# Performance work log

Measured on AMD Instinct MI355X. Metric: run time of the kernel, lower is better.

The kernel has to match this reference:

```python
import jax, jax.numpy as jnp
import numpy as np

N = 384      # max_nodes
H = 256      # layers[0] == layers[1] == layers[2]
Z = 128      # dim_z
ED = 128     # edge_dim
AH = ED // 2 # attention hidden

# complete directed graph: combinations (i<j) then reversed pairs
_i, _j = np.triu_indices(N, k=1)
_SRC = jnp.asarray(np.concatenate([_i, _j]), dtype=jnp.int32)  # edge_index[0]
_DST = jnp.asarray(np.concatenate([_j, _i]), dtype=jnp.int32)  # edge_index[1]


def setup_inputs() -> dict:
    key = jax.random.key(0)
    ks = jax.random.split(key, 16)
    def p(k, shape, fan_in):
        return jax.random.normal(k, shape, dtype=jnp.float32) * (1.0 / np.sqrt(fan_in))
    return {
        "z": jax.random.normal(ks[0], (1, Z), dtype=jnp.float32),
        # GRU (torch layout: W_ih [3H, Z], W_hh [3H, H]; gate order r, z, n)
        "gru_Wih": p(ks[1], (3 * H, Z), Z),
        "gru_Whh": p(ks[2], (3 * H, H), H),
        "gru_bih": jnp.zeros((3 * H,), jnp.float32),
        "gru_bhh": jnp.zeros((3 * H,), jnp.float32),
        # edge_generator MLP: 2H -> 4H -> ED
        "eg_W1": p(ks[3], (2 * H, 4 * H), 2 * H), "eg_b1": jnp.zeros((4 * H,), jnp.float32),
        "eg_W2": p(ks[4], (4 * H, ED), 4 * H),   "eg_b2": jnp.zeros((ED,), jnp.float32),
        # attention MLPs: (ED+H) -> ED//2 -> 1
        "att0_W1": p(ks[5], (ED + H, AH), ED + H), "att0_b1": jnp.zeros((AH,), jnp.float32),
        "att0_W2": p(ks[6], (AH, 1), AH),           "att0_b2": jnp.zeros((1,), jnp.float32),
        "att1_W1": p(ks[7], (ED + H, AH), ED + H), "att1_b1": jnp.zeros((AH,), jnp.float32),
        "att1_W2": p(ks[8], (AH, 1), AH),           "att1_b2": jnp.zeros((1,), jnp.float32),
        # EdgeConv output linears: H -> H
        "conv0_W": p(ks[9], (H, H), H),  "conv0_b": jnp.zeros((H,), jnp.float32),
        "conv1_W": p(ks[10], (H, H), H), "conv1_b": jnp.zeros((H,), jnp.float32),
    }


def _forward(z, gru_Wih, gru_Whh, gru_bih, gru_bhh,
             eg_W1, eg_b1, eg_W2, eg_b2,
             att0_W1, att0_b1, att0_W2, att0_b2,
             att1_W1, att1_b1, att1_W2, att1_b2,
             conv0_W, conv0_b, conv1_W, conv1_b):
    # --- GRU node generation: input is the same latent z at every step ---
    gi = z[0] @ gru_Wih.T + gru_bih            # [3H], constant per step
    gir, giz, gin = jnp.split(gi, 3)
    def step(h, _):
        gh = h @ gru_Whh.T + gru_bhh
        ghr, ghz, ghn = jnp.split(gh, 3)
        r = jax.nn.sigmoid(gir + ghr)
        u = jax.nn.sigmoid(giz + ghz)
        n = jnp.tanh(gin + r * ghn)
        h2 = (1.0 - u) * n + u * h
        return h2, h2
    _, nodes = jax.lax.scan(step, jnp.zeros((H,), z.dtype), None, length=N)  # [N, H]

    # --- edge features over the complete directed graph ---
    pairs = jnp.concatenate([nodes[_SRC], nodes[_DST]], axis=-1)            # [E, 2H]
    edges = jax.nn.relu(pairs @ eg_W1 + eg_b1) @ eg_W2 + eg_b2              # [E, ED]

    # --- EdgeConv: gather src, attention MLP gate, scatter-sum, linear ---
    def conv(x, aW1, ab1, aW2, ab2, W, b):
        xs = x[_SRC]                                                        # [E, H]
        a_in = jnp.concatenate([edges, xs], axis=-1)                        # [E, ED+H]
        att = jax.nn.sigmoid(jax.nn.relu(a_in @ aW1 + ab1) @ aW2 + ab2)     # [E, 1]
        agg = jax.ops.segment_sum(att * xs, _DST, num_segments=N)           # [N, H]
        return agg @ W + b

    x = jax.nn.relu(conv(nodes, att0_W1, att0_b1, att0_W2, att0_b2, conv0_W, conv0_b))
    x = conv(x, att1_W1, att1_b1, att1_W2, att1_b2, conv1_W, conv1_b)
    return jnp.sum(x, axis=0)                                               # [H]


def reference(z, gru_Wih, gru_Whh, gru_bih, gru_bhh,
              eg_W1, eg_b1, eg_W2, eg_b2,
              att0_W1, att0_b1, att0_W2, att0_b2,
              att1_W1, att1_b1, att1_W2, att1_b2,
              conv0_W, conv0_b, conv1_W, conv1_b):
    return _forward(z, gru_Wih, gru_Whh, gru_bih, gru_bhh,
                    eg_W1, eg_b1, eg_W2, eg_b2,
                    att0_W1, att0_b1, att0_W2, att0_b2,
                    att1_W1, att1_b1, att1_W2, att1_b2,
                    conv0_W, conv0_b, conv1_W, conv1_b)
```

## Files before the change

### kernel.cpp

```cpp
#include <hip/hip_runtime.h>
#include <hip/hip_fp16.h>
#include <cstdint>

#define DEV static __device__ __forceinline__

typedef _Float16 h2v __attribute__((ext_vector_type(2)));
typedef _Float16 half8 __attribute__((ext_vector_type(8)));
typedef float float4v __attribute__((ext_vector_type(4)));

union U32H2 { uint32_t u; _Float16 f[2]; };

DEV uint32_t pack_f2(float a, float b) {
    auto p = __builtin_amdgcn_cvt_pkrtz(a, b);
    return __builtin_bit_cast(uint32_t, p);
}

DEV half8 bc8(uint4 v) { return __builtin_bit_cast(half8, v); }

DEV void gl_lds16(const void* gsrc, void* ldst) {
    __builtin_amdgcn_global_load_lds(
        (const __attribute__((address_space(1))) uint32_t*)gsrc,
        (__attribute__((address_space(3))) uint32_t*)ldst, 16, 0, 0);
}

DEV float pick4(float4v lo, float4v hi, int bsel, int r) {
    float v0 = bsel ? hi[0] : lo[0];
    float v1 = bsel ? hi[1] : lo[1];
    float v2 = bsel ? hi[2] : lo[2];
    float v3 = bsel ? hi[3] : lo[3];
    float x01 = (r & 1) ? v1 : v0;
    float x23 = (r & 1) ? v3 : v2;
    return (r & 2) ? x23 : x01;
}

static const size_t OFF_W16T  = 0;
static const size_t OFF_GI    = 98304;
static const size_t OFF_CC    = 99072;
static const size_t OFF_BF    = 99200;
static const size_t OFF_NODES = 164736;
static const size_t OFF_PF    = 263040;
static const size_t OFF_QF    = 459648;
static const size_t OFF_R0    = 656256;
static const size_t OFF_R1    = 680832;
static const size_t OFF_TT    = 705408;
static const size_t OFF_ATT0  = 10142592;
static const size_t OFF_ATT1  = 10290048;
static const size_t OFF_AGG   = 10437504;
static const size_t OFF_X0    = 10535808;
static const size_t OFF_CS    = 10634112;
static const size_t WS_TOTAL  = 10634816;

__global__ void k_prep_wl(const float* __restrict__ Whh, uint32_t* __restrict__ WL,
                          const float* __restrict__ z, const float* __restrict__ Wih,
                          const float* __restrict__ bih, const float* __restrict__ bhh,
                          float* __restrict__ gs) {
    int bb = blockIdx.x, tid = threadIdx.x;
    if (bb < 48) {
        int c = bb;
        int rt = c >> 3, kt = c & 7;
        int lane = tid & 63, wv = tid >> 6;
        int row = (rt >> 1) * 256 + wv * 32 + ((rt & 1) << 4) + (lane & 15);
        int k0 = kt*32 + (lane >> 4)*8;
        const float* src = Whh + row*256 + k0;
        uint4 o;
        o.x = pack_f2(src[0], src[1]);
        o.y = pack_f2(src[2], src[3]);
        o.z = pack_f2(src[4], src[5]);
        o.w = pack_f2(src[6], src[7]);
        ((uint4*)WL)[c*512 + tid] = o;
    } else {
        int o = (bb - 48) * 512 + tid;
        if (o < 768) {
            float acc = bih[o];
            if (o < 512) acc += bhh[o];
            for (int i = 0; i < 128; ++i) acc += Wih[o*128 + i] * z[i];
            gs[o] = acc;
        }
    }
}

__global__ void __launch_bounds__(512, 2)
k_gru_bf(const float* __restrict__ gs, const float* __restrict__ bhh,
         const uint32_t* __restrict__ WL, float* __restrict__ nodes,
         const float* __restrict__ egW2, const float* __restrict__ egb2,
         const float* __restrict__ a0W1, const float* __restrict__ a1W1,
         uint32_t* __restrict__ BF, float* __restrict__ cc) {
    int bb = blockIdx.x, tid = threadIdx.x;
    if (bb == 0) {
        __shared__ __align__(16) _Float16 hh16[512];
        int lane = tid & 63, wv = tid >> 6;
        int kq = lane >> 4, c = lane & 15;
        const float L2E = 1.44269504088896f;
        int r = c & 3, bsel = (c >> 2) & 1;
        int gidx = wv*32 + kq*4 + r + bsel*16;
        bool active = (c < 8);

        uint4 w[48];
        const uint4* wl4 = (const uint4*)WL;
        #pragma unroll
        for (int q = 0; q < 48; ++q) w[q] = wl4[q*512 + tid];
        #pragma unroll
        for (int q = 0; q < 48; ++q)
            asm volatile("" : "+a"(w[q].x), "+a"(w[q].y), "+a"(w[q].z), "+a"(w[q].w));

        float pr = -L2E * gs[gidx];
        float pz = -L2E * gs[256 + gidx];
        float pn = -2.f * L2E * gs[512 + gidx];
        float bn_l = bhh[512 + gidx];

        float h = 0.f;
        if (tid < 256) ((uint32_t*)hh16)[tid] = 0u;
        __syncthreads();

        const float4v z4 = {0.f, 0.f, 0.f, 0.f};
        int par = 0;
        for (int t = 0; t < 384; ++t) {
            const _Float16* hb = hh16 + par*256 + kq*8;
            uint4 b[8];
            #pragma unroll
            for (int kt = 0; kt < 8; ++kt) b[kt] = *(const uint4*)(hb + kt*32);

            float4v d0, d1, d2, d3, d4, d5;
            d0 = __builtin_amdgcn_mfma_f32_16x16x32_f16(bc8(w[0]),  bc8(b[0]), z4, 0, 0, 0);
            d1 = __builtin_amdgcn_mfma_f32_16x16x32_f16(bc8(w[8]),  bc8(b[0]), z4, 0, 0, 0);
            #pragma unroll
            for (int kt = 1; kt < 8; ++kt) {
                d0 = __builtin_amdgcn_mfma_f32_16x16x32_f16(bc8(w[kt]),   bc8(b[kt]), d0, 0, 0, 0);
                d1 = __builtin_amdgcn_mfma_f32_16x16x32_f16(bc8(w[8+kt]), bc8(b[kt]), d1, 0, 0, 0);
            }
            float ghr = pick4(d0, d1, bsel, r);
            float er = __builtin_amdgcn_exp2f(__builtin_fmaf(ghr, -L2E, pr));
            float rg = __builtin_amdgcn_rcpf(1.f + er);

            d2 = __builtin_amdgcn_mfma_f32_16x16x32_f16(bc8(w[16]), bc8(b[0]), z4, 0, 0, 0);
            d3 = __builtin_amdgcn_mfma_f32_16x16x32_f16(bc8(w[24]), bc8(b[0]), z4, 0, 0, 0);
            d4 = __builtin_amdgcn_mfma_f32_16x16x32_f16(bc8(w[32]), bc8(b[0]), z4, 0, 0, 0);
            d5 = __builtin_amdgcn_mfma_f32_16x16x32_f16(bc8(w[40]), bc8(b[0]), z4, 0, 0, 0);
            #pragma unroll
            for (int kt = 1; kt < 8; ++kt) {
                d2 = __builtin_amdgcn_mfma_f32_16x16x32_f16(bc8(w[16+kt]), bc8(b[kt]), d2, 0, 0, 0);
                d3 = __builtin_amdgcn_mfma_f32_16x16x32_f16(bc8(w[24+kt]), bc8(b[kt]), d3, 0, 0, 0);
                d4 = __builtin_amdgcn_mfma_f32_16x16x32_f16(bc8(w[32+kt]), bc8(b[kt]), d4, 0, 0, 0);
                d5 = __builtin_amdgcn_mfma_f32_16x16x32_f16(bc8(w[40+kt]), bc8(b[kt]), d5, 0, 0, 0);
            }

            float ghz = pick4(d2, d3, bsel, r);
            float ghn = pick4(d4, d5, bsel, r);
            float eu = __builtin_amdgcn_exp2f(__builtin_fmaf(ghz, -L2E, pz));
            float u  = __builtin_amdgcn_rcpf(1.f + eu);
            float tm = ghn + bn_l;
            float q  = __builtin_fmaf(rg * tm, -2.f * L2E, pn);
            float e2 = __builtin_amdgcn_exp2f(q);
            float nn = __builtin_fmaf(2.f, __builtin_amdgcn_rcpf(1.f + e2), -1.f);
            h = nn + u * (h - nn);

            if (active) {
                hh16[(par ^ 1)*256 + gidx] = (_Float16)h;
                nodes[t*256 + gidx] = h;
            }
            asm volatile("s_waitcnt lgkmcnt(0)" ::: "memory");
            __builtin_amdgcn_sched_barrier(0);
            __builtin_amdgcn_s_barrier();
            __builtin_amdgcn_sched_barrier(0);
            par ^= 1;
        }
    } else if (bb < 129) {
        int idx = (bb - 1) * 512 + tid;
        int k2 = idx >> 7, n = idx & 127;
        const float* A = (n < 64) ? (a0W1 + n) : (a1W1 + (n - 64));
        const float* w0 = egW2 + (2*k2) * 128;
        float a = 0.f, b = 0.f;
        for (int i = 0; i < 128; ++i) {
            float av = A[i*64];
            a += w0[i] * av;
            b += w0[128 + i] * av;
        }
        int kk = k2 >> 4, jgrp = (k2 >> 2) & 3, sub = k2 & 3;
        int lane = jgrp*16 + (n & 15), t = n >> 4;
        BF[((kk*8 + t)*64 + lane)*4 + sub] = pack_f2(a, b);
    } else {
        if (tid < 128) {
            const float* A = (tid < 64) ? a0W1 : a1W1;
            int j = tid & 63;
            float acc = 0.f;
            for (int i = 0; i < 128; ++i) acc += egb2[i] * A[i*64 + j];
            cc[tid] = acc;
        }
    }
}

__global__ void k_pq(const float* __restrict__ nodes, const float* __restrict__ eg_W1,
                     const float* __restrict__ eg_b1, const float* __restrict__ a0W1,
                     const float* __restrict__ a0b1, const float* __restrict__ cc,
                     uint32_t* __restrict__ PF, uint32_t* __restrict__ QF,
                     float* __restrict__ R0) {
    int tid = threadIdx.x;
    int s0 = blockIdx.x * 4;
    __shared__ float ns[4][256];
    #pragma unroll
    for (int q = 0; q < 4; ++q) ns[q][tid] = nodes[(s0+q)*256 + tid];
    __syncthreads();

    int k0 = tid * 4;
    float acc[4][4];
    #pragma unroll
    for (int q = 0; q < 4; ++q) { acc[q][0]=0;acc[q][1]=0;acc[q][2]=0;acc[q][3]=0; }
    for (int i = 0; i < 256; ++i) {
        float4 wv = *(const float4*)&eg_W1[i*1024 + k0];
        #pragma unroll
        for (int q = 0; q < 4; ++q) {
            float nv = ns[q][i];
            acc[q][0] += nv*wv.x; acc[q][1] += nv*wv.y;
            acc[q][2] += nv*wv.z; acc[q][3] += nv*wv.w;
        }
    }
    float4 bv = *(const float4*)&eg_b1[k0];
    {
        int kk = k0 >> 5;
        int lgrp = ((k0 >> 3) & 3) * 16;
        int sub = (k0 & 7) >> 1;
        #pragma unroll
        for (int q = 0; q < 4; ++q) {
            int s = s0 + q, g = s >> 4, srow = s & 15;
            uint2 pw;
            pw.x = pack_f2(acc[q][0] + bv.x, acc[q][1] + bv.y);
            pw.y = pack_f2(acc[q][2] + bv.z, acc[q][3] + bv.w);
            *(uint2*)(PF + (((g*32 + kk)*64 + lgrp + srow) << 2) + sub) = pw;
        }
    }

    #pragma unroll
    for (int q = 0; q < 4; ++q) { acc[q][0]=0;acc[q][1]=0;acc[q][2]=0;acc[q][3]=0; }
    for (int i = 0; i < 256; ++i) {
        float4 wv = *(const float4*)&eg_W1[(256+i)*1024 + k0];
        #pragma unroll
        for (int q = 0; q < 4; ++q) {
            float nv = ns[q][i];
            acc[q][0] += nv*wv.x; acc[q][1] += nv*wv.y;
            acc[q][2] += nv*wv.z; acc[q][3] += nv*wv.w;
        }
    }
    #pragma unroll
    for (int q = 0; q < 4; ++q) {
        uint2 pw;
        pw.x = pack_f2(acc[q][0], acc[q][1]);
        pw.y = pack_f2(acc[q][2], acc[q][3]);
        ((uint2*)QF)[(s0+q)*256 + tid] = pw;
    }

    int srow = tid >> 6, j = tid & 63;
    float racc = a0b1[j] + cc[j];
    for (int i = 0; i < 256; ++i) racc += ns[srow][i] * a0W1[(128+i)*64 + j];
    R0[(s0+srow)*64 + j] = racc;
}

__global__ void __launch_bounds__(512, 4)
k_phaseA(const uint32_t* __restrict__ PF, const uint32_t* __restrict__ QF,
         const uint32_t* __restrict__ BF, const float* __restrict__ R0,
         const float* __restrict__ a0W2, const float* __restrict__ a0b2,
         uint32_t* __restrict__ TT, float* __restrict__ ATT0) {
    __shared__ __align__(16) char smem[69632];
    uint4* Qs4 = (uint4*)smem;
    char* bufbase = smem + 32768;
    int tid = threadIdx.x;
    int lane = tid & 63, wv = tid >> 6;
    int g = blockIdx.x, dt = blockIdx.y, d0 = dt * 16;

    {
        const char* src = (const char*)(QF + (size_t)d0 * 512);
        for (int off = tid*16; off < 32768; off += 8192)
            gl_lds16(src + off, (char*)Qs4 + off);
    }
    {
        const char* psrc = (const char*)(PF + (size_t)g * 8192);
        if (tid < 128) gl_lds16(psrc + tid*16, bufbase + tid*16);
        const char* bsrc = (const char*)BF;
        #pragma unroll
        for (int i = 0; i < 2; ++i)
            gl_lds16(bsrc + tid*16 + i*8192, bufbase + 2048 + tid*16 + i*8192);
    }
    asm volatile("s_waitcnt vmcnt(0)" ::: "memory");
    __builtin_amdgcn_sched_barrier(0);
    __builtin_amdgcn_s_barrier();
    __builtin_amdgcn_sched_barrier(0);

    float4v acc[2][8];
    #pragma unroll
    for (int t = 0; t < 2; ++t)
        #pragma unroll
        for (int n = 0; n < 8; ++n) acc[t][n] = 0.f;

    for (int hc = 0; hc < 16; ++hc) {
        char* cur = bufbase + (hc & 1) * 18432;
        char* nxt = bufbase + ((hc + 1) & 1) * 18432;
        if (hc < 15) {
            const char* psrc = (const char*)(PF + ((size_t)g*32 + (size_t)(hc+1)*2) * 256);
            if (tid < 128) gl_lds16(psrc + tid*16, nxt + tid*16);
            const char* bsrc = (const char*)(BF + (size_t)(hc+1) * 4096);
            #pragma unroll
            for (int i = 0; i < 2; ++i)
                gl_lds16(bsrc + tid*16 + i*8192, nxt + 2048 + tid*16 + i*8192);
        }
        uint4* Ph = (uint4*)cur;
        uint4* Bh = (uint4*)(cur + 2048);
        #pragma unroll
        for (int kkl = 0; kkl < 2; ++kkl) {
            int kkg = hc*2 + kkl;
            half8 b[8];
            #pragma unroll
            for (int n = 0; n < 8; ++n) b[n] = bc8(Bh[(kkl*8 + n)*64 + lane]);
            half8 p8 = bc8(Ph[kkl*64 + lane]);
            #pragma unroll
            for (int t = 0; t < 2; ++t) {
                half8 q8 = bc8(Qs4[(wv*2 + t)*128 + kkg*4 + (lane >> 4)]);
                half8 x = p8 + q8;
                half8 zz = 0;
                x = __builtin_elementwise_max(x, zz);
                #pragma unroll
                for (int n = 0; n < 8; ++n)
                    acc[t][n] = __builtin_amdgcn_mfma_f32_16x16x32_f16(x, b[n], acc[t][n], 0, 0, 0);
            }
        }
        asm volatile("s_waitcnt vmcnt(0)" ::: "memory");
        __builtin_amdgcn_sched_barrier(0);
        __builtin_amdgcn_s_barrier();
        __builtin_amdgcn_sched_barrier(0);
    }

    __syncthreads();
    float* R0s = (float*)smem;
    float* w2s = (float*)(smem + 4096);
    for (int i = tid; i < 1024; i += 512)
        R0s[i] = R0[(size_t)(g*16 + (i >> 6))*64 + (i & 63)];
    if (tid < 64) w2s[tid] = a0W2[tid];
    float b2v = a0b2[0];

    _Float16* epi = (_Float16*)(smem + 32768);
    int cn = lane & 15, rhi = (lane >> 4) * 4;
    for (int half = 0; half < 2; ++half) {
        __syncthreads();
        #pragma unroll
        for (int t = 0; t < 2; ++t) {
            int dl = wv*2 + t;
            #pragma unroll
            for (int n = 0; n < 4; ++n) {
                int j = n*16 + cn;
                float4v v = acc[t][half*4 + n];
                #pragma unroll
                for (int r = 0; r < 4; ++r)
                    epi[((rhi + r)*16 + dl)*64 + j] = (_Float16)v[r];
            }
        }
        __syncthreads();
        {
            int p = tid >> 1, sub = tid & 1;
            int srow = p >> 4, dl = p & 15;
            const uint4* src = (const uint4*)(epi + (size_t)p*64);
            uint4* dst = (uint4*)(TT + ((size_t)((g*16 + srow)*384 + d0 + dl))*64 + half*32);
            #pragma unroll
            for (int q = 0; q < 4; ++q) dst[sub*4 + q] = src[sub*4 + q];
        }
        if (half == 0 && tid < 256) {
            int sl = tid >> 4, dl = tid & 15;
            const _Float16* tp = epi + (size_t)(sl*16 + dl)*64;
            const float* rp = R0s + sl*64;
            float logit = b2v;
            #pragma unroll
            for (int j = 0; j < 64; ++j)
                logit += fmaxf((float)tp[j] + rp[j], 0.f) * w2s[j];
            float a = 1.f / (1.f + __expf(-logit));
            int s = g*16 + sl, d = d0 + dl;
            ATT0[(size_t)s*384 + d] = (s == d) ? 0.f : a;
        }
    }
}

__global__ void k_att(const uint32_t* __restrict__ TT, const float* __restrict__ R,
                      const float* __restrict__ w2, const float* __restrict__ b2,
                      int off, float* __restrict__ ATT, float* __restrict__ CS) {
    int tid = threadIdx.x;
    int p = blockIdx.x * 256 + tid;
    int s = p / 384, d = p - s * 384;
    int sa = (blockIdx.x * 256) / 384;
    __shared__ float w2s[64];
    __shared__ float rs[2][64];
    if (tid < 64) w2s[tid] = w2[tid];
    else if (tid < 128) rs[0][tid - 64] = R[sa*64 + (tid - 64)];
    else if (tid < 192) {
        int sb = sa + 1;
        rs[1][tid - 128] = (sb < 384) ? R[sb*64 + (tid - 128)] : 0.f;
    }
    __syncthreads();
    const uint4* tp = (const uint4*)(TT + (size_t)p*64 + off);
    const float* rp = (s == sa) ? rs[0] : rs[1];
    float logit = b2[0];
    #pragma unroll
    for (int m = 0; m < 8; ++m) {
        uint4 tv = tp[m];
        uint32_t us[4] = {tv.x, tv.y, tv.z, tv.w};
        #pragma unroll
        for (int q = 0; q < 4; ++q) {
            U32H2 c; c.u = us[q];
            int j = m*8 + q*2;
            float h0 = fmaxf((float)c.f[0] + rp[j],   0.f);
            float h1 = fmaxf((float)c.f[1] + rp[j+1], 0.f);
            logit += h0*w2s[j] + h1*w2s[j+1];
        }
    }
    float a = 1.f / (1.f + __expf(-logit));
    float a_eff = (s == d) ? 0.f : a;
    ATT[p] = a_eff;

    if (CS) {
        float va = (s == sa) ? a_eff : 0.f;
        float vb = (s != sa) ? a_eff : 0.f;
        #pragma unroll
        for (int o = 32; o > 0; o >>= 1) {
            va += __shfl_down(va, o, 64);
            vb += __shfl_down(vb, o, 64);
        }
        if ((tid & 63) == 0) {
            atomicAdd(&CS[sa], va);
            int sb = sa + 1;
            if (sb < 384) atomicAdd(&CS[sb], vb);
        }
    }
}

__global__ void __launch_bounds__(256)
k_aggx0(const float* __restrict__ ATT, const float* __restrict__ X,
        const float* __restrict__ W, const float* __restrict__ b,
        const float* __restrict__ a1W1, const float* __restrict__ a1b1,
        const float* __restrict__ cc,
        float* __restrict__ X0, float* __restrict__ R1) {
    int d = blockIdx.x, tid = threadIdx.x;
    __shared__ float att_col[384];
    __shared__ float ag[256];
    __shared__ float xs[256];
    for (int s = tid; s < 384; s += 256) att_col[s] = ATT[(size_t)s*384 + d];
    __syncthreads();
    float acc = 0.f;
    #pragma unroll 4
    for (int s = 0; s < 384; ++s)
        acc += att_col[s] * X[(size_t)s*256 + tid];
    ag[tid] = acc;
    __syncthreads();
    float x0 = b[tid];
    for (int i = 0; i < 256; ++i) x0 += ag[i] * W[i*256 + tid];
    x0 = fmaxf(x0, 0.f);
    X0[(size_t)d*256 + tid] = x0;
    xs[tid] = x0;
    __syncthreads();
    if (tid < 64) {
        float r = a1b1[tid] + cc[64 + tid];
        for (int i = 0; i < 256; ++i) r += xs[i] * a1W1[(128+i)*64 + tid];
        R1[(size_t)d*64 + tid] = r;
    }
}

__global__ void k_vout(const float* __restrict__ CS, const float* __restrict__ X0,
                       const float* __restrict__ W, const float* __restrict__ b,
                       float* __restrict__ out) {
    int tid = threadIdx.x;
    __shared__ float cs[384];
    __shared__ float vs[256];
    for (int q = tid; q < 384; q += 256) cs[q] = CS[q];
    __syncthreads();
    float acc = 0.f;
    for (int s = 0; s < 384; s += 4) {
        acc += cs[s]*X0[s*256 + tid] + cs[s+1]*X0[(s+1)*256 + tid]
             + cs[s+2]*X0[(s+2)*256 + tid] + cs[s+3]*X0[(s+3)*256 + tid];
    }
    vs[tid] = acc;
    __syncthreads();
    float o = 384.f * b[tid];
    for (int i = 0; i < 256; ++i) o += vs[i] * W[i*256 + tid];
    out[tid] = o;
}

extern "C" void kernel_launch(void* const* d_in, const int* in_sizes, int n_in,
                              void* d_out, int out_size, void* d_ws, size_t ws_size,
                              hipStream_t stream) {
    if (ws_size < WS_TOTAL * sizeof(uint32_t)) return;

    const float* z    = (const float*)d_in[0];
    const float* Wih  = (const float*)d_in[1];
    const float* Whh  = (const float*)d_in[2];
    const float* bih  = (const float*)d_in[3];
    const float* bhh  = (const float*)d_in[4];
    const float* egW1 = (const float*)d_in[5];
    const float* egb1 = (const float*)d_in[6];
    const float* egW2 = (const float*)d_in[7];
    const float* egb2 = (const float*)d_in[8];
    const float* a0W1 = (const float*)d_in[9];
    const float* a0b1 = (const float*)d_in[10];
    const float* a0W2 = (const float*)d_in[11];
    const float* a0b2 = (const float*)d_in[12];
    const float* a1W1 = (const float*)d_in[13];
    const float* a1b1 = (const float*)d_in[14];
    const float* a1W2 = (const float*)d_in[15];
    const float* a1b2 = (const float*)d_in[16];
    const float* c0W  = (const float*)d_in[17];
    const float* c0b  = (const float*)d_in[18];
    const float* c1W  = (const float*)d_in[19];
    const float* c1b  = (const float*)d_in[20];

    uint32_t* ws   = (uint32_t*)d_ws;
    uint32_t* WL   = ws + OFF_W16T;
    float*    gs   = (float*)(ws + OFF_GI);
    float*    cc   = (float*)(ws + OFF_CC);
    uint32_t* BF   = ws + OFF_BF;
    float*    nodes= (float*)(ws + OFF_NODES);
    uint32_t* PF   = ws + OFF_PF;
    uint32_t* QF   = ws + OFF_QF;
    float*    R0   = (float*)(ws + OFF_R0);
    float*    R1   = (float*)(ws + OFF_R1);
    uint32_t* TT   = ws + OFF_TT;
    float*    ATT0 = (float*)(ws + OFF_ATT0);
    float*    ATT1 = (float*)(ws + OFF_ATT1);
    float*    X0   = (float*)(ws + OFF_X0);
    float*    CS   = (float*)(ws + OFF_CS);
    float*    out  = (float*)d_out;

    hipMemsetAsync(CS, 0, 384 * sizeof(float), stream);
    hipLaunchKernelGGL(k_prep_wl, dim3(50),     dim3(512), 0, stream, Whh, WL, z, Wih, bih, bhh, gs);
    hipLaunchKernelGGL(k_gru_bf,  dim3(130),    dim3(512), 0, stream, gs, bhh, WL, nodes,
                       egW2, egb2, a0W1, a1W1, BF, cc);
    hipLaunchKernelGGL(k_pq,      dim3(96),     dim3(256), 0, stream, nodes, egW1, egb1, a0W1, a0b1, cc, PF, QF, R0);
    hipLaunchKernelGGL(k_phaseA,  dim3(24, 24), dim3(512), 0, stream, PF, QF, BF, R0, a0W2, a0b2, TT, ATT0);
    hipLaunchKernelGGL(k_aggx0,   dim3(384),    dim3(256), 0, stream, ATT0, nodes, c0W, c0b, a1W1, a1b1, cc, X0, R1);
    hipLaunchKernelGGL(k_att,     dim3(576),    dim3(256), 0, stream, TT, R1, a1W2, a1b2, 32, ATT1, CS);
    hipLaunchKernelGGL(k_vout,    dim3(1),      dim3(256), 0, stream, CS, X0, c1W, c1b, out);
}
```

Before: 668.9 us.

## Replace MFMA GRU recurrence matvec with packed fdot2 and quad shuffle reduction

The sequential 384-step GRU loop used 16x16x32 MFMAs for a single-vector matvec, wasting most of the tile and needing select logic to pick outputs. It now has each thread hold 192 packed fp16 weight pairs in VGPRs and compute partial dot products for two hidden units with v_dot2. The four threads covering one unit pair then combine their partials with xor shuffles. The weight prep kernel is relaid out to match. This aims to shorten per-step latency on the serial critical path, but adds register pressure and shuffle latency.

```diff
diff --git a/kernel.cpp b/kernel.cpp
--- a/kernel.cpp
+++ b/kernel.cpp
@@ -16,6 +16,11 @@
 }
 
 DEV half8 bc8(uint4 v) { return __builtin_bit_cast(half8, v); }
+
+DEV float fdot2(uint32_t a, uint32_t b, float c) {
+    return __builtin_amdgcn_fdot2(__builtin_bit_cast(h2v, a),
+                                  __builtin_bit_cast(h2v, b), c, false);
+}
 
 DEV void gl_lds16(const void* gsrc, void* ldst) {
     __builtin_amdgcn_global_load_lds(
@@ -23,17 +28,7 @@
         (__attribute__((address_space(3))) uint32_t*)ldst, 16, 0, 0);
 }
 
-DEV float pick4(float4v lo, float4v hi, int bsel, int r) {
-    float v0 = bsel ? hi[0] : lo[0];
-    float v1 = bsel ? hi[1] : lo[1];
-    float v2 = bsel ? hi[2] : lo[2];
-    float v3 = bsel ? hi[3] : lo[3];
-    float x01 = (r & 1) ? v1 : v0;
-    float x23 = (r & 1) ? v3 : v2;
-    return (r & 2) ? x23 : x01;
-}
-
-static const size_t OFF_W16T  = 0;
+static const size_t OFF_WV    = 0;
 static const size_t OFF_GI    = 98304;
 static const size_t OFF_CC    = 99072;
 static const size_t OFF_BF    = 99200;
@@ -45,31 +40,27 @@
 static const size_t OFF_TT    = 705408;
 static const size_t OFF_ATT0  = 10142592;
 static const size_t OFF_ATT1  = 10290048;
-static const size_t OFF_AGG   = 10437504;
 static const size_t OFF_X0    = 10535808;
 static const size_t OFF_CS    = 10634112;
 static const size_t WS_TOTAL  = 10634816;
 
-__global__ void k_prep_wl(const float* __restrict__ Whh, uint32_t* __restrict__ WL,
+__global__ void k_prep_wl(const float* __restrict__ Whh, uint32_t* __restrict__ WV,
                           const float* __restrict__ z, const float* __restrict__ Wih,
                           const float* __restrict__ bih, const float* __restrict__ bhh,
                           float* __restrict__ gs) {
     int bb = blockIdx.x, tid = threadIdx.x;
-    if (bb < 48) {
-        int c = bb;
-        int rt = c >> 3, kt = c & 7;
-        int lane = tid & 63, wv = tid >> 6;
-        int row = (rt >> 1) * 256 + wv * 32 + ((rt & 1) << 4) + (lane & 15);
-        int k0 = kt*32 + (lane >> 4)*8;
-        const float* src = Whh + row*256 + k0;
-        uint4 o;
-        o.x = pack_f2(src[0], src[1]);
-        o.y = pack_f2(src[2], src[3]);
-        o.z = pack_f2(src[4], src[5]);
-        o.w = pack_f2(src[6], src[7]);
-        ((uint4*)WL)[c*512 + tid] = o;
+    if (bb < 192) {
+        int j = bb;
+        int i = j >> 5, jj = j & 31;
+        int e0 = 2 * (tid >> 2);
+        int e = e0 + (i >= 3 ? 1 : 0);
+        int g = (i >= 3) ? i - 3 : i;
+        int row = 256*g + e;
+        int k = (tid & 3)*64 + 2*jj;
+        const float* src = Whh + (size_t)row*256 + k;
+        WV[(size_t)j*512 + tid] = pack_f2(src[0], src[1]);
     } else {
-        int o = (bb - 48) * 512 + tid;
+        int o = (bb - 192) * 512 + tid;
         if (o < 768) {
             float acc = bih[o];
             if (o < 512) acc += bhh[o];
@@ -81,82 +72,83 @@
 
 __global__ void __launch_bounds__(512, 2)
 k_gru_bf(const float* __restrict__ gs, const float* __restrict__ bhh,
-         const uint32_t* __restrict__ WL, float* __restrict__ nodes,
+         const uint32_t* __restrict__ WV, float* __restrict__ nodes,
          const float* __restrict__ egW2, const float* __restrict__ egb2,
          const float* __restrict__ a0W1, const float* __restrict__ a1W1,
          uint32_t* __restrict__ BF, float* __restrict__ cc) {
     int bb = blockIdx.x, tid = threadIdx.x;
     if (bb == 0) {
         __shared__ __align__(16) _Float16 hh16[512];
-        int lane = tid & 63, wv = tid >> 6;
-        int kq = lane >> 4, c = lane & 15;
         const float L2E = 1.44269504088896f;
-        int r = c & 3, bsel = (c >> 2) & 1;
-        int gidx = wv*32 + kq*4 + r + bsel*16;
-        bool active = (c < 8);
-
-        uint4 w[48];
-        const uint4* wl4 = (const uint4*)WL;
-        #pragma unroll
-        for (int q = 0; q < 48; ++q) w[q] = wl4[q*512 + tid];
-        #pragma unroll
-        for (int q = 0; q < 48; ++q)
-            asm volatile("" : "+a"(w[q].x), "+a"(w[q].y), "+a"(w[q].z), "+a"(w[q].w));
-
-        float pr = -L2E * gs[gidx];
-        float pz = -L2E * gs[256 + gidx];
-        float pn = -2.f * L2E * gs[512 + gidx];
-        float bn_l = bhh[512 + gidx];
-
-        float h = 0.f;
+        int e0 = 2 * (tid >> 2);
+        int e1 = e0 + 1;
+        int ks = (tid & 3) * 64;
+        bool writer = (tid & 3) == 0;
+
+        uint32_t w[6][32];
+        #pragma unroll
+        for (int i = 0; i < 6; ++i)
+            #pragma unroll
+            for (int j = 0; j < 32; ++j)
+                w[i][j] = WV[(size_t)(i*32 + j)*512 + tid];
+
+        float pr0 = -L2E * gs[e0],        pr1 = -L2E * gs[e1];
+        float pz0 = -L2E * gs[256 + e0],  pz1 = -L2E * gs[256 + e1];
+        float pn0 = -2.f * L2E * gs[512 + e0];
+        float pn1 = -2.f * L2E * gs[512 + e1];
+        float bn0 = bhh[512 + e0],        bn1 = bhh[512 + e1];
+
+        float h0 = 0.f, h1 = 0.f;
         if (tid < 256) ((uint32_t*)hh16)[tid] = 0u;
         __syncthreads();
 
-        const float4v z4 = {0.f, 0.f, 0.f, 0.f};
         int par = 0;
         for (int t = 0; t < 384; ++t) {
-            const _Float16* hb = hh16 + par*256 + kq*8;
-            uint4 b[8];
-            #pragma unroll
-            for (int kt = 0; kt < 8; ++kt) b[kt] = *(const uint4*)(hb + kt*32);
-
-            float4v d0, d1, d2, d3, d4, d5;
-            d0 = __builtin_amdgcn_mfma_f32_16x16x32_f16(bc8(w[0]),  bc8(b[0]), z4, 0, 0, 0);
-            d1 = __builtin_amdgcn_mfma_f32_16x16x32_f16(bc8(w[8]),  bc8(b[0]), z4, 0, 0, 0);
-            #pragma unroll
-            for (int kt = 1; kt < 8; ++kt) {
-                d0 = __builtin_amdgcn_mfma_f32_16x16x32_f16(bc8(w[kt]),   bc8(b[kt]), d0, 0, 0, 0);
-                d1 = __builtin_amdgcn_mfma_f32_16x16x32_f16(bc8(w[8+kt]), bc8(b[kt]), d1, 0, 0, 0);
+            const uint4* hb = (const uint4*)(hh16 + par*256 + ks);
+            float a0 = 0.f, a1 = 0.f, a2 = 0.f, a3 = 0.f, a4 = 0.f, a5 = 0.f;
+            #pragma unroll
+            for (int m = 0; m < 8; ++m) {
+                uint4 hv = hb[m];
+                uint32_t hu[4] = {hv.x, hv.y, hv.z, hv.w};
+                #pragma unroll
+                for (int c = 0; c < 4; ++c) {
+                    int j = 4*m + c;
+                    a0 = fdot2(w[0][j], hu[c], a0);
+                    a1 = fdot2(w[1][j], hu[c], a1);
+                    a2 = fdot2(w[2][j], hu[c], a2);
+                    a3 = fdot2(w[3][j], hu[c], a3);
+                    a4 = fdot2(w[4][j], hu[c], a4);
+                    a5 = fdot2(w[5][j], hu[c], a5);
+                }
             }
-            float ghr = pick4(d0, d1, bsel, r);
-            float er = __builtin_amdgcn_exp2f(__builtin_fmaf(ghr, -L2E, pr));
-            float rg = __builtin_amdgcn_rcpf(1.f + er);
-
-            d2 = __builtin_amdgcn_mfma_f32_16x16x32_f16(bc8(w[16]), bc8(b[0]), z4, 0, 0, 0);
-            d3 = __builtin_amdgcn_mfma_f32_16x16x32_f16(bc8(w[24]), bc8(b[0]), z4, 0, 0, 0);
-            d4 = __builtin_amdgcn_mfma_f32_16x16x32_f16(bc8(w[32]), bc8(b[0]), z4, 0, 0, 0);
-            d5 = __builtin_amdgcn_mfma_f32_16x16x32_f16(bc8(w[40]), bc8(b[0]), z4, 0, 0, 0);
-            #pragma unroll
-            for (int kt = 1; kt < 8; ++kt) {
-                d2 = __builtin_amdgcn_mfma_f32_16x16x32_f16(bc8(w[16+kt]), bc8(b[kt]), d2, 0, 0, 0);
-                d3 = __builtin_amdgcn_mfma_f32_16x16x32_f16(bc8(w[24+kt]), bc8(b[kt]), d3, 0, 0, 0);
-                d4 = __builtin_amdgcn_mfma_f32_16x16x32_f16(bc8(w[32+kt]), bc8(b[kt]), d4, 0, 0, 0);
-                d5 = __builtin_amdgcn_mfma_f32_16x16x32_f16(bc8(w[40+kt]), bc8(b[kt]), d5, 0, 0, 0);
-            }
-
-            float ghz = pick4(d2, d3, bsel, r);
-            float ghn = pick4(d4, d5, bsel, r);
-            float eu = __builtin_amdgcn_exp2f(__builtin_fmaf(ghz, -L2E, pz));
-            float u  = __builtin_amdgcn_rcpf(1.f + eu);
-            float tm = ghn + bn_l;
-            float q  = __builtin_fmaf(rg * tm, -2.f * L2E, pn);
-            float e2 = __builtin_amdgcn_exp2f(q);
-            float nn = __builtin_fmaf(2.f, __builtin_amdgcn_rcpf(1.f + e2), -1.f);
-            h = nn + u * (h - nn);
-
-            if (active) {
-                hh16[(par ^ 1)*256 + gidx] = (_Float16)h;
-                nodes[t*256 + gidx] = h;
+            a0 += __shfl_xor(a0, 1, 64); a0 += __shfl_xor(a0, 2, 64);
+            a1 += __shfl_xor(a1, 1, 64); a1 += __shfl_xor(a1, 2, 64);
+            a2 += __shfl_xor(a2, 1, 64); a2 += __shfl_xor(a2, 2, 64);
+            a3 += __shfl_xor(a3, 1, 64); a3 += __shfl_xor(a3, 2, 64);
+            a4 += __shfl_xor(a4, 1, 64); a4 += __shfl_xor(a4, 2, 64);
+            a5 += __shfl_xor(a5, 1, 64); a5 += __shfl_xor(a5, 2, 64);
+
+            float er0 = __builtin_amdgcn_exp2f(__builtin_fmaf(a0, -L2E, pr0));
+            float rg0 = __builtin_amdgcn_rcpf(1.f + er0);
+            float eu0 = __builtin_amdgcn_exp2f(__builtin_fmaf(a1, -L2E, pz0));
+            float u0  = __builtin_amdgcn_rcpf(1.f + eu0);
+            float q0  = __builtin_fmaf(rg0 * (a2 + bn0), -2.f * L2E, pn0);
+            float e20 = __builtin_amdgcn_exp2f(q0);
+            float nn0 = __builtin_fmaf(2.f, __builtin_amdgcn_rcpf(1.f + e20), -1.f);
+            h0 = nn0 + u0 * (h0 - nn0);
+
+            float er1 = __builtin_amdgcn_exp2f(__builtin_fmaf(a3, -L2E, pr1));
+            float rg1 = __builtin_amdgcn_rcpf(1.f + er1);
+            float eu1 = __builtin_amdgcn_exp2f(__builtin_fmaf(a4, -L2E, pz1));
+            float u1  = __builtin_amdgcn_rcpf(1.f + eu1);
+            float q1  = __builtin_fmaf(rg1 * (a5 + bn1), -2.f * L2E, pn1);
+            float e21 = __builtin_amdgcn_exp2f(q1);
+            float nn1 = __builtin_fmaf(2.f, __builtin_amdgcn_rcpf(1.f + e21), -1.f);
+            h1 = nn1 + u1 * (h1 - nn1);
+
+            if (writer) {
+                ((uint32_t*)hh16)[(par ^ 1)*128 + (e0 >> 1)] = pack_f2(h0, h1);
+                *(float2*)(nodes + (size_t)t*256 + e0) = make_float2(h0, h1);
             }
             asm volatile("s_waitcnt lgkmcnt(0)" ::: "memory");
             __builtin_amdgcn_sched_barrier(0);
@@ -506,7 +498,7 @@
     const float* c1b  = (const float*)d_in[20];
 
     uint32_t* ws   = (uint32_t*)d_ws;
-    uint32_t* WL   = ws + OFF_W16T;
+    uint32_t* WV   = ws + OFF_WV;
     float*    gs   = (float*)(ws + OFF_GI);
     float*    cc   = (float*)(ws + OFF_CC);
     uint32_t* BF   = ws + OFF_BF;
@@ -523,8 +515,8 @@
     float*    out  = (float*)d_out;
 
     hipMemsetAsync(CS, 0, 384 * sizeof(float), stream);
-    hipLaunchKernelGGL(k_prep_wl, dim3(50),     dim3(512), 0, stream, Whh, WL, z, Wih, bih, bhh, gs);
-    hipLaunchKernelGGL(k_gru_bf,  dim3(130),    dim3(512), 0, stream, gs, bhh, WL, nodes,
+    hipLaunchKernelGGL(k_prep_wl, dim3(194),    dim3(512), 0, stream, Whh, WV, z, Wih, bih, bhh, gs);
+    hipLaunchKernelGGL(k_gru_bf,  dim3(130),    dim3(512), 0, stream, gs, bhh, WV, nodes,
                        egW2, egb2, a0W1, a1W1, BF, cc);
     hipLaunchKernelGGL(k_pq,      dim3(96),     dim3(256), 0, stream, nodes, egW1, egb1, a0W1, a0b1, cc, PF, QF, R0);
     hipLaunchKernelGGL(k_phaseA,  dim3(24, 24), dim3(512), 0, stream, PF, QF, BF, R0, a0W2, a0b2, TT, ATT0);
```

Result: slower. 718.2 us (+7.4%).

## Fuse GRU weight prep into GRU kernel, drop memset, store only needed TT half

Applied to the files above, without the earlier changes.

Removes the separate weight-packing/input-projection kernel: the GRU block now packs Whh to fp16 fragments and computes the z projection itself. The CS memset is folded into the aggregation kernel, and phaseA writes only the second half of the edge features to TT, which halves that intermediate's footprint. This cuts two launches and a large chunk of global write traffic. The trade-off is that the serial GRU block now does the packing and matvec on its critical path.

```diff
diff --git a/kernel.cpp b/kernel.cpp
--- a/kernel.cpp
+++ b/kernel.cpp
@@ -45,49 +45,21 @@
 static const size_t OFF_TT    = 705408;
 static const size_t OFF_ATT0  = 10142592;
 static const size_t OFF_ATT1  = 10290048;
-static const size_t OFF_AGG   = 10437504;
 static const size_t OFF_X0    = 10535808;
 static const size_t OFF_CS    = 10634112;
 static const size_t WS_TOTAL  = 10634816;
 
-__global__ void k_prep_wl(const float* __restrict__ Whh, uint32_t* __restrict__ WL,
-                          const float* __restrict__ z, const float* __restrict__ Wih,
-                          const float* __restrict__ bih, const float* __restrict__ bhh,
-                          float* __restrict__ gs) {
-    int bb = blockIdx.x, tid = threadIdx.x;
-    if (bb < 48) {
-        int c = bb;
-        int rt = c >> 3, kt = c & 7;
-        int lane = tid & 63, wv = tid >> 6;
-        int row = (rt >> 1) * 256 + wv * 32 + ((rt & 1) << 4) + (lane & 15);
-        int k0 = kt*32 + (lane >> 4)*8;
-        const float* src = Whh + row*256 + k0;
-        uint4 o;
-        o.x = pack_f2(src[0], src[1]);
-        o.y = pack_f2(src[2], src[3]);
-        o.z = pack_f2(src[4], src[5]);
-        o.w = pack_f2(src[6], src[7]);
-        ((uint4*)WL)[c*512 + tid] = o;
-    } else {
-        int o = (bb - 48) * 512 + tid;
-        if (o < 768) {
-            float acc = bih[o];
-            if (o < 512) acc += bhh[o];
-            for (int i = 0; i < 128; ++i) acc += Wih[o*128 + i] * z[i];
-            gs[o] = acc;
-        }
-    }
-}
-
 __global__ void __launch_bounds__(512, 2)
-k_gru_bf(const float* __restrict__ gs, const float* __restrict__ bhh,
-         const uint32_t* __restrict__ WL, float* __restrict__ nodes,
+k_gru_bf(const float* __restrict__ Whh, const float* __restrict__ z,
+         const float* __restrict__ Wih, const float* __restrict__ bih,
+         const float* __restrict__ bhh, float* __restrict__ nodes,
          const float* __restrict__ egW2, const float* __restrict__ egb2,
          const float* __restrict__ a0W1, const float* __restrict__ a1W1,
          uint32_t* __restrict__ BF, float* __restrict__ cc) {
     int bb = blockIdx.x, tid = threadIdx.x;
     if (bb == 0) {
         __shared__ __align__(16) _Float16 hh16[512];
+        __shared__ float zs[128];
         int lane = tid & 63, wv = tid >> 6;
         int kq = lane >> 4, c = lane & 15;
         const float L2E = 1.44269504088896f;
@@ -96,20 +68,47 @@
         bool active = (c < 8);
 
         uint4 w[48];
-        const uint4* wl4 = (const uint4*)WL;
-        #pragma unroll
-        for (int q = 0; q < 48; ++q) w[q] = wl4[q*512 + tid];
-        #pragma unroll
-        for (int q = 0; q < 48; ++q)
-            asm volatile("" : "+a"(w[q].x), "+a"(w[q].y), "+a"(w[q].z), "+a"(w[q].w));
-
-        float pr = -L2E * gs[gidx];
-        float pz = -L2E * gs[256 + gidx];
-        float pn = -2.f * L2E * gs[512 + gidx];
+        #pragma unroll
+        for (int cidx = 0; cidx < 48; ++cidx) {
+            int rt = cidx >> 3, kt = cidx & 7;
+            int row = (rt >> 1) * 256 + wv * 32 + ((rt & 1) << 4) + (lane & 15);
+            int k0 = kt*32 + (lane >> 4)*8;
+            const float* src = Whh + (size_t)row*256 + k0;
+            uint4 o;
+            o.x = pack_f2(src[0], src[1]);
+            o.y = pack_f2(src[2], src[3]);
+            o.z = pack_f2(src[4], src[5]);
+            o.w = pack_f2(src[6], src[7]);
+            w[cidx] = o;
+        }
+        #pragma unroll
+        for (int cidx = 0; cidx < 48; ++cidx)
+            asm volatile("" : "+a"(w[cidx].x), "+a"(w[cidx].y), "+a"(w[cidx].z), "+a"(w[cidx].w));
+
+        if (tid < 128) zs[tid] = z[tid];
+        if (tid < 256) ((uint32_t*)hh16)[tid] = 0u;
+        __syncthreads();
+        float s_r = bih[gidx] + bhh[gidx];
+        float s_z = bih[256 + gidx] + bhh[256 + gidx];
+        float s_n = bih[512 + gidx];
+        {
+            const float4* wr = (const float4*)(Wih + (size_t)gidx*128);
+            const float4* wzp = (const float4*)(Wih + (size_t)(256+gidx)*128);
+            const float4* wn = (const float4*)(Wih + (size_t)(512+gidx)*128);
+            for (int i = 0; i < 32; ++i) {
+                float4 zv = ((const float4*)zs)[i];
+                float4 a = wr[i], b = wzp[i], d = wn[i];
+                s_r += a.x*zv.x + a.y*zv.y + a.z*zv.z + a.w*zv.w;
+                s_z += b.x*zv.x + b.y*zv.y + b.z*zv.z + b.w*zv.w;
+                s_n += d.x*zv.x + d.y*zv.y + d.z*zv.z + d.w*zv.w;
+            }
+        }
+        float pr = -L2E * s_r;
+        float pz = -L2E * s_z;
+        float pn = -2.f * L2E * s_n;
         float bn_l = bhh[512 + gidx];
 
         float h = 0.f;
-        if (tid < 256) ((uint32_t*)hh16)[tid] = 0u;
         __syncthreads();
 
         const float4v z4 = {0.f, 0.f, 0.f, 0.f};
@@ -352,11 +351,11 @@
             }
         }
         __syncthreads();
-        {
+        if (half == 1) {
             int p = tid >> 1, sub = tid & 1;
             int srow = p >> 4, dl = p & 15;
             const uint4* src = (const uint4*)(epi + (size_t)p*64);
-            uint4* dst = (uint4*)(TT + ((size_t)((g*16 + srow)*384 + d0 + dl))*64 + half*32);
+            uint4* dst = (uint4*)(TT + ((size_t)((g*16 + srow)*384 + d0 + dl))*32);
             #pragma unroll
             for (int q = 0; q < 4; ++q) dst[sub*4 + q] = src[sub*4 + q];
         }
@@ -377,7 +376,7 @@
 
 __global__ void k_att(const uint32_t* __restrict__ TT, const float* __restrict__ R,
                       const float* __restrict__ w2, const float* __restrict__ b2,
-                      int off, float* __restrict__ ATT, float* __restrict__ CS) {
+                      float* __restrict__ ATT, float* __restrict__ CS) {
     int tid = threadIdx.x;
     int p = blockIdx.x * 256 + tid;
     int s = p / 384, d = p - s * 384;
@@ -391,7 +390,7 @@
         rs[1][tid - 128] = (sb < 384) ? R[sb*64 + (tid - 128)] : 0.f;
     }
     __syncthreads();
-    const uint4* tp = (const uint4*)(TT + (size_t)p*64 + off);
+    const uint4* tp = (const uint4*)(TT + (size_t)p*32);
     const float* rp = (s == sa) ? rs[0] : rs[1];
     float logit = b2[0];
     #pragma unroll
@@ -411,19 +410,17 @@
     float a_eff = (s == d) ? 0.f : a;
     ATT[p] = a_eff;
 
-    if (CS) {
-        float va = (s == sa) ? a_eff : 0.f;
-        float vb = (s != sa) ? a_eff : 0.f;
-        #pragma unroll
-        for (int o = 32; o > 0; o >>= 1) {
-            va += __shfl_down(va, o, 64);
-            vb += __shfl_down(vb, o, 64);
-        }
-        if ((tid & 63) == 0) {
-            atomicAdd(&CS[sa], va);
-            int sb = sa + 1;
-            if (sb < 384) atomicAdd(&CS[sb], vb);
-        }
+    float va = (s == sa) ? a_eff : 0.f;
+    float vb = (s != sa) ? a_eff : 0.f;
+    #pragma unroll
+    for (int o = 32; o > 0; o >>= 1) {
+        va += __shfl_down(va, o, 64);
+        vb += __shfl_down(vb, o, 64);
+    }
+    if ((tid & 63) == 0) {
+        atomicAdd(&CS[sa], va);
+        int sb = sa + 1;
+        if (sb < 384) atomicAdd(&CS[sb], vb);
     }
 }
 
@@ -432,8 +429,11 @@
         const float* __restrict__ W, const float* __restrict__ b,
         const float* __restrict__ a1W1, const float* __restrict__ a1b1,
         const float* __restrict__ cc,
-        float* __restrict__ X0, float* __restrict__ R1) {
+        float* __restrict__ X0, float* __restrict__ R1, float* __restrict__ CS) {
     int d = blockIdx.x, tid = threadIdx.x;
+    if (d == 0) {
+        for (int s = tid; s < 384; s += 256) CS[s] = 0.f;
+    }
     __shared__ float att_col[384];
     __shared__ float ag[256];
     __shared__ float xs[256];
@@ -506,8 +506,6 @@
     const float* c1b  = (const float*)d_in[20];
 
     uint32_t* ws   = (uint32_t*)d_ws;
-    uint32_t* WL   = ws + OFF_W16T;
-    float*    gs   = (float*)(ws + OFF_GI);
     float*    cc   = (float*)(ws + OFF_CC);
     uint32_t* BF   = ws + OFF_BF;
     float*    nodes= (float*)(ws + OFF_NODES);
@@ -522,13 +520,11 @@
     float*    CS   = (float*)(ws + OFF_CS);
     float*    out  = (float*)d_out;
 
-    hipMemsetAsync(CS, 0, 384 * sizeof(float), stream);
-    hipLaunchKernelGGL(k_prep_wl, dim3(50),     dim3(512), 0, stream, Whh, WL, z, Wih, bih, bhh, gs);
-    hipLaunchKernelGGL(k_gru_bf,  dim3(130),    dim3(512), 0, stream, gs, bhh, WL, nodes,
-                       egW2, egb2, a0W1, a1W1, BF, cc);
+    hipLaunchKernelGGL(k_gru_bf,  dim3(130),    dim3(512), 0, stream,
+                       Whh, z, Wih, bih, bhh, nodes, egW2, egb2, a0W1, a1W1, BF, cc);
     hipLaunchKernelGGL(k_pq,      dim3(96),     dim3(256), 0, stream, nodes, egW1, egb1, a0W1, a0b1, cc, PF, QF, R0);
     hipLaunchKernelGGL(k_phaseA,  dim3(24, 24), dim3(512), 0, stream, PF, QF, BF, R0, a0W2, a0b2, TT, ATT0);
-    hipLaunchKernelGGL(k_aggx0,   dim3(384),    dim3(256), 0, stream, ATT0, nodes, c0W, c0b, a1W1, a1b1, cc, X0, R1);
-    hipLaunchKernelGGL(k_att,     dim3(576),    dim3(256), 0, stream, TT, R1, a1W2, a1b2, 32, ATT1, CS);
+    hipLaunchKernelGGL(k_aggx0,   dim3(384),    dim3(256), 0, stream, ATT0, nodes, c0W, c0b, a1W1, a1b1, cc, X0, R1, CS);
+    hipLaunchKernelGGL(k_att,     dim3(576),    dim3(256), 0, stream, TT, R1, a1W2, a1b2, ATT1, CS);
     hipLaunchKernelGGL(k_vout,    dim3(1),      dim3(256), 0, stream, CS, X0, c1W, c1b, out);
 }
```

Result: slower. 1.268 ms (+89.5%).
